# Optimization experiments

Measured on AMD Instinct MI355X. Metric: run time of the kernel, lower is better.

The kernel has to match this reference:

```python
import jax, jax.numpy as jnp
import numpy as np

N_NODES = 100000
N_EDGES = 800000


def gcn_conv(x, W, b, src, dst, ew, n):
    # PyG GCNConv with edge weights and self-loops already included in (src, dst, ew):
    # deg[i] = sum of incoming edge weights at i; norm_e = d^-1/2[src] * w_e * d^-1/2[dst]
    h = x @ W                                                  # [N, F_out]
    deg = jax.ops.segment_sum(ew, dst, num_segments=n)         # [N]
    dinv = jnp.where(deg > 0, jax.lax.rsqrt(deg), 0.0)
    norm = dinv[src] * ew * dinv[dst]                          # [E]
    out = jax.ops.segment_sum(h[src] * norm[:, None], dst, num_segments=n)
    return out + b


def add_self_loops(edge_index, edge_weight, n):
    loop = jnp.arange(n, dtype=edge_index.dtype)
    src = jnp.concatenate([edge_index[0], loop])
    dst = jnp.concatenate([edge_index[1], loop])
    ew = jnp.concatenate([edge_weight, jnp.ones((n,), edge_weight.dtype)])
    return src, dst, ew


def setup_inputs() -> dict:
    key = jax.random.key(0)
    ks = jax.random.split(key, 10)
    x = jax.random.normal(ks[0], (N_NODES, 5), jnp.float32)
    edge_index = jax.random.randint(ks[1], (2, N_EDGES), 0, N_NODES, dtype=jnp.int64)
    edge_weight = jax.random.uniform(ks[2], (N_EDGES,), jnp.float32)
    def glorot(k, fan_in, fan_out):
        s = float(np.sqrt(6.0 / (fan_in + fan_out)))
        return jax.random.uniform(k, (fan_in, fan_out), jnp.float32, -s, s)
    return {
        "x": x,
        "edge_index": edge_index,
        "edge_weight": edge_weight,
        "W1": glorot(ks[3], 5, 320),
        "b1": jnp.zeros((320,), jnp.float32),
        "W2": glorot(ks[4], 320, 160),
        "b2": jnp.zeros((160,), jnp.float32),
        "We": glorot(ks[5], 160, 80),
        "be": jnp.zeros((80,), jnp.float32),
    }


def reference(x, edge_index, edge_weight, W1, b1, W2, b2, We, be):
    n = x.shape[0]
    src, dst, ew = add_self_loops(edge_index, edge_weight, n)
    h = gcn_conv(x, W1, b1, src, dst, ew, n)        # conv1
    h = jax.nn.relu(h)
    h = gcn_conv(h, W2, b2, src, dst, ew, n)        # conv2
    return h @ We + be                              # embed linear
```

## Files before the change

kernel.cpp:

```cpp
#include <hip/hip_runtime.h>

#define NF0 5
#define F1 320
#define F2 160
#define F3 80
#define NSUB 8
#define SUBCAP 512

typedef float f32x4 __attribute__((ext_vector_type(4)));
typedef _Float16 f16x8 __attribute__((ext_vector_type(8)));


__global__ void k_init(int* __restrict__ zreg, int zwords,
                       const unsigned int* __restrict__ ei32, int E, int* __restrict__ flag) {
    for (int t = blockIdx.x * 256 + threadIdx.x; t < zwords; t += gridDim.x * 256)
        zreg[t] = 0;
    if (blockIdx.x == 0) {
        __shared__ int ok;
        if (threadIdx.x == 0) ok = 1;
        __syncthreads();
        int np = E < 2048 ? E : 2048;
        for (int i = threadIdx.x; i < np; i += 256)
            if (ei32[2 * i + 1] != 0u) ok = 0;
        __syncthreads();
        if (threadIdx.x == 0) *flag = ok;
    }
}


__global__ void k_binA(const void* ei, const float* __restrict__ ew, const int* __restrict__ flag,
                       int* __restrict__ bin_cnt , int2* __restrict__ bins,
                       int n_bins, int* __restrict__ ovf_n, int* __restrict__ ovf,
                       int ovf_cap, int E) {
    int e = blockIdx.x * blockDim.x + threadIdx.x;
    if (e >= E) return;
    int sub = blockIdx.x & (NSUB - 1);
    int s, d;
    if (*flag) {
        const long long* p = (const long long*)ei;
        s = (int)p[e]; d = (int)p[E + e];
    } else {
        const int* p = (const int*)ei;
        s = p[e]; d = p[E + e];
    }
    float w = ew[e];
    int b = d >> 8;
    int pos = atomicAdd(&bin_cnt[(sub * n_bins + b) * 4], 1);
    if (pos < SUBCAP) {
        int2 pk;
        pk.x = s | ((d & 255) << 24);
        pk.y = __float_as_int(w);
        bins[(size_t)b * (NSUB * SUBCAP) + sub * SUBCAP + pos] = pk;
    } else {
        int o = atomicAdd(ovf_n, 1);
        if (o < ovf_cap) {
            ovf[3 * o] = s; ovf[3 * o + 1] = d; ovf[3 * o + 2] = __float_as_int(w);
        }
    }
}


__global__ __launch_bounds__(512) void k_binB1x(const int2* __restrict__ bins,
                                                const int* __restrict__ bin_cnt, int n_bins,
                                                float* __restrict__ dinv,
                                                const int* __restrict__ ovf_n,
                                                const int* __restrict__ ovf, int ovf_cap, int N,
                                                const float* __restrict__ W2,
                                                const float* __restrict__ We,
                                                _Float16* __restrict__ Bh,
                                                const float* __restrict__ b2,
                                                const float* __restrict__ be,
                                                float* __restrict__ bc) {
    __shared__ float deg_l[256];
    int b = blockIdx.x, t = threadIdx.x;
    if (b >= n_bins) {
        int xb = b - n_bins;
        if (xb < 50) {
            int idx = xb * 512 + t;
            int fid = idx >> 9;
            int rem = idx & 511;
            int lane = rem >> 3, i = rem & 7;
            int kk = fid / 5, ct = fid - kk * 5;
            int col = ct * 16 + (lane & 15);
            int row = kk * 32 + (lane >> 4) * 8 + i;
            const float* wr = W2 + (size_t)row * F2;
            float acc = 0.f;
            #pragma unroll 4
            for (int m = 0; m < F2; m += 4) {
                float4 w4 = *(const float4*)(wr + m);
                acc += w4.x * We[m * F3 + col] + w4.y * We[(m + 1) * F3 + col]
                     + w4.z * We[(m + 2) * F3 + col] + w4.w * We[(m + 3) * F3 + col];
            }
            Bh[((size_t)fid * 64 + lane) * 8 + i] = (_Float16)acc;
        } else {
            if (t < F3) {
                float s = be[t];
                for (int k = 0; k < F2; ++k) s += b2[k] * We[k * F3 + t];
                bc[t] = s;
            }
        }
        return;
    }
    if (t < 256) deg_l[t] = 0.f;
    __syncthreads();
    int th = t >> 8;
    int tt = t & 255;
    for (int sp = 0; sp < NSUB; sp += 2) {
        int sub = sp + th;
        int ne = bin_cnt[(sub * n_bins + b) * 4]; if (ne > SUBCAP) ne = SUBCAP;
        const int2* bp = bins + (size_t)b * (NSUB * SUBCAP) + sub * SUBCAP;
        for (int j = tt; j < ne; j += 256) {
            int2 pk = bp[j];
            atomicAdd(&deg_l[((unsigned int)pk.x) >> 24], __int_as_float(pk.y));
        }
    }
    int n = *ovf_n; if (n > ovf_cap) n = ovf_cap;
    int lo = b * 256;
    for (int j = t; j < n; j += 512) {
        int d = ovf[3 * j + 1];
        if (d >= lo && d < lo + 256)
            atomicAdd(&deg_l[d - lo], __int_as_float(ovf[3 * j + 2]));
    }
    __syncthreads();
    int node = lo + t;
    if (t < 256 && node < N) dinv[node] = rsqrtf(1.0f + deg_l[t]);
}


__global__ __launch_bounds__(512) void k_binB2node(const int2* __restrict__ bins,
                                                   const int* __restrict__ bin_cnt, int n_bins,
                                                   const float* __restrict__ dinv,
                                                   const float* __restrict__ x,
                                                   const float* __restrict__ W1,
                                                   const float* __restrict__ b1,
                                                   const _Float16* __restrict__ Bh,
                                                   int* __restrict__ cnt,
                                                   int2* __restrict__ bucket, int cap,
                                                   int* __restrict__ ovf_n, int* __restrict__ ovf,
                                                   int ovf_cap,
                                                   _Float16* __restrict__ g, int N) {
    __shared__ int cnt_l[256];
    __shared__ float acc_l[256 * NF0];
    __shared__ float W_l[6 * F1];
    __shared__ _Float16 B_l[50 * 64 * 8];
    int b = blockIdx.x, t = threadIdx.x;

    if (t < 480) {
        float4 v = (t < 400) ? ((const float4*)W1)[t] : ((const float4*)b1)[t - 400];
        ((float4*)W_l)[t] = v;
    }
    {
        const float4* src = (const float4*)Bh;
        float4* dst = (float4*)B_l;
        for (int i = t; i < 3200; i += 512) dst[i] = src[i];
    }
    if (t < 256) cnt_l[t] = 0;
    for (int q = t; q < 256 * NF0; q += 512) acc_l[q] = 0.f;
    int nsnap = *ovf_n; if (nsnap > ovf_cap) nsnap = ovf_cap;
    __syncthreads();
    int lo = b * 256;

    for (int j = t; j < nsnap; j += 512) {
        int d = ovf[3 * j + 1];
        if (d >= lo && d < lo + 256) {
            int s = ovf[3 * j];
            float w = __int_as_float(ovf[3 * j + 2]) * dinv[s];
            const float* xs = x + (size_t)s * NF0;
            int dl = d - lo;
            #pragma unroll
            for (int f = 0; f < NF0; ++f)
                atomicAdd(&acc_l[dl * NF0 + f], xs[f] * w);
        }
    }

    int th = t >> 8;
    int tt = t & 255;
    for (int sp = 0; sp < NSUB; sp += 2) {
        int sub = sp + th;
        int ne = bin_cnt[(sub * n_bins + b) * 4]; if (ne > SUBCAP) ne = SUBCAP;
        const int2* bp = bins + (size_t)b * (NSUB * SUBCAP) + sub * SUBCAP;
        for (int j = tt; j < ne; j += 256) {
            int2 pk = bp[j];
            int s = pk.x & 0xFFFFFF;
            int dl = ((unsigned int)pk.x) >> 24;
            int node = lo + dl;
            int pos = atomicAdd(&cnt_l[dl], 1);
            if (pos < cap) {
                int2 out_pk; out_pk.x = s; out_pk.y = pk.y;
                bucket[(size_t)node * cap + pos] = out_pk;
            } else {
                int o = atomicAdd(ovf_n, 1);
                if (o < ovf_cap) { ovf[3 * o] = s; ovf[3 * o + 1] = node; ovf[3 * o + 2] = pk.y; }
            }
            float w = __int_as_float(pk.y) * dinv[s];
            const float* xs = x + (size_t)s * NF0;
            float4 sv = *(const float4*)xs;
            float s4 = xs[4];
            atomicAdd(&acc_l[dl * NF0 + 0], sv.x * w);
            atomicAdd(&acc_l[dl * NF0 + 1], sv.y * w);
            atomicAdd(&acc_l[dl * NF0 + 2], sv.z * w);
            atomicAdd(&acc_l[dl * NF0 + 3], sv.w * w);
            atomicAdd(&acc_l[dl * NF0 + 4], s4 * w);
        }
    }
    __syncthreads();

    int node0 = lo + t;
    if (t < 256 && node0 < N) {
        float di = dinv[node0];
        float sc = di * di;
        const float* xn = x + (size_t)node0 * NF0;
        #pragma unroll
        for (int f = 0; f < NF0; ++f)
            acc_l[t * NF0 + f] = di * acc_l[t * NF0 + f] + sc * xn[f];
        int c = cnt_l[t]; if (c > cap) c = cap;
        cnt[node0] = c;
    }
    __syncthreads();

    int w = t >> 6, l = t & 63;
    int nl = l & 15, kg = l >> 4;
    f32x4 zero = {0.f, 0.f, 0.f, 0.f};
    const f16x8* blp = (const f16x8*)B_l;

    #pragma unroll
    for (int set = 0; set < 2; ++set) {
        int nlocal = w * 32 + set * 16 + nl;
        int base = lo + w * 32 + set * 16;
        float a0v[5];
        #pragma unroll
        for (int j = 0; j < 5; ++j) a0v[j] = acc_l[nlocal * NF0 + j];

        f32x4 acc[5] = {zero, zero, zero, zero, zero};
        #pragma unroll
        for (int kk = 0; kk < 10; ++kk) {
            int k0 = kk * 32 + kg * 8;
            float v0[8];
            const float* bb = W_l + 5 * F1 + k0;
            #pragma unroll
            for (int i = 0; i < 8; ++i) v0[i] = bb[i];
            #pragma unroll
            for (int j = 0; j < 5; ++j) {
                const float* wp = W_l + j * F1 + k0;
                float aj0 = a0v[j];
                #pragma unroll
                for (int i = 0; i < 8; ++i) v0[i] += aj0 * wp[i];
            }
            f16x8 ah0;
            #pragma unroll
            for (int i = 0; i < 8; ++i)
                ah0[i] = (_Float16)fmaxf(v0[i], 0.f);
            #pragma unroll
            for (int ct = 0; ct < 5; ++ct) {
                f16x8 bf = blp[(kk * 5 + ct) * 64 + l];
                acc[ct] = __builtin_amdgcn_mfma_f32_16x16x32_f16(ah0, bf, acc[ct], 0, 0, 0);
            }
        }

        #pragma unroll
        for (int r = 0; r < 4; ++r) {
            int r0 = base + kg * 4 + r;
            if (r0 < N) {
                float dv = dinv[r0];
                #pragma unroll
                for (int ct = 0; ct < 5; ++ct)
                    g[(size_t)r0 * F3 + ct * 16 + nl] = (_Float16)(acc[ct][r] * dv);
            }
        }
    }
}


__global__ __launch_bounds__(256) void k_aggB(const _Float16* __restrict__ g,
                                              const float* __restrict__ dinv,
                                              const float* __restrict__ bc,
                                              const int* __restrict__ cnt,
                                              const int2* __restrict__ bucket, int cap,
                                              float* __restrict__ out, int N) {
    int t = blockIdx.x * blockDim.x + threadIdx.x;
    if (t >= 10 * N) return;
    int i = t / 10;
    int c = (t - i * 10) << 3;
    float acc[8];
    #pragma unroll
    for (int e = 0; e < 8; ++e) acc[e] = 0.f;
    int cn = cnt[i];
    const int4* row4 = (const int4*)(bucket + (size_t)i * cap);
    int j = 0;
    for (; j + 2 <= cn; j += 2) {
        int4 q = row4[j >> 1];
        float w0 = __int_as_float(q.y);
        float w1 = __int_as_float(q.w);
        f16x8 a0 = *(const f16x8*)(g + (size_t)q.x * F3 + c);
        f16x8 a1 = *(const f16x8*)(g + (size_t)q.z * F3 + c);
        #pragma unroll
        for (int e = 0; e < 8; ++e)
            acc[e] += (float)a0[e] * w0 + (float)a1[e] * w1;
    }
    if (j < cn) {
        int2 p0 = ((const int2*)row4)[j];
        float w0 = __int_as_float(p0.y);
        f16x8 a0 = *(const f16x8*)(g + (size_t)p0.x * F3 + c);
        #pragma unroll
        for (int e = 0; e < 8; ++e)
            acc[e] += (float)a0[e] * w0;
    }
    float di = dinv[i];
    f16x8 u0 = *(const f16x8*)(g + (size_t)i * F3 + c);
    const f32x4* bp = (const f32x4*)(bc + c);
    f32x4 q0 = bp[0], q1 = bp[1];
    f32x4 o0, o1;
    o0.x = di * (acc[0] + (float)u0[0]) + q0.x;
    o0.y = di * (acc[1] + (float)u0[1]) + q0.y;
    o0.z = di * (acc[2] + (float)u0[2]) + q0.z;
    o0.w = di * (acc[3] + (float)u0[3]) + q0.w;
    o1.x = di * (acc[4] + (float)u0[4]) + q1.x;
    o1.y = di * (acc[5] + (float)u0[5]) + q1.y;
    o1.z = di * (acc[6] + (float)u0[6]) + q1.z;
    o1.w = di * (acc[7] + (float)u0[7]) + q1.w;
    f32x4* op = (f32x4*)(out + (size_t)i * F3 + c);
    __builtin_nontemporal_store(o0, op);
    __builtin_nontemporal_store(o1, op + 1);
}

__global__ void k_fixB(const _Float16* __restrict__ g, const float* __restrict__ dinv,
                       const int* __restrict__ ovf_n, const int* __restrict__ ovf, int ovf_cap,
                       float* __restrict__ out) {
    int n = *ovf_n; if (n > ovf_cap) n = ovf_cap;
    for (int j = blockIdx.x * blockDim.x + threadIdx.x; j < n; j += gridDim.x * blockDim.x) {
        int s = ovf[3 * j], d = ovf[3 * j + 1];
        float w = dinv[d] * __int_as_float(ovf[3 * j + 2]);
        for (int f = 0; f < F3; ++f)
            atomicAdd(&out[(size_t)d * F3 + f], (float)g[(size_t)s * F3 + f] * w);
    }
}


static inline size_t align256(size_t x) { return (x + 255) & ~(size_t)255; }

extern "C" void kernel_launch(void* const* d_in, const int* in_sizes, int n_in,
                              void* d_out, int out_size, void* d_ws, size_t ws_size,
                              hipStream_t stream) {
    const float* x  = (const float*)d_in[0];
    const void*  ei = d_in[1];
    const float* ew = (const float*)d_in[2];
    const float* W1 = (const float*)d_in[3];
    const float* b1 = (const float*)d_in[4];
    const float* W2 = (const float*)d_in[5];
    const float* b2 = (const float*)d_in[6];
    const float* We = (const float*)d_in[7];
    const float* be = (const float*)d_in[8];
    float* out = (float*)d_out;

    int N = in_sizes[0] / NF0;
    int E = in_sizes[2];

    const int OVF_CAP = 131072;
    int n_bins = (N + 255) >> 8;

    char* p = (char*)d_ws;
    auto alloc = [&](size_t bytes) { char* r = p; p += align256(bytes); return r; };
    int*   flag  = (int*)alloc(4);
    int zwords = 16 + NSUB * n_bins * 4;
    int*   zreg  = (int*)alloc((size_t)zwords * 4);
    int*   ovf_n = zreg;
    int*   bin_cnt = zreg + 16;
    float* dinv  = (float*)alloc((size_t)N * 4);
    int*   cnt   = (int*)  alloc((size_t)N * 4);
    int*   ovf   = (int*)  alloc((size_t)OVF_CAP * 12);
    int2*  bins  = (int2*) alloc((size_t)n_bins * NSUB * SUBCAP * 8);
    float* bc    = (float*)alloc((size_t)F3 * 4);
    _Float16* Bh = (_Float16*)alloc((size_t)50 * 64 * 8 * 2);
    _Float16* g  = (_Float16*)alloc((size_t)N * F3 * 2);

    size_t used = (size_t)(p - (char*)d_ws);
    int cap = 24;
    if (ws_size > used) {
        size_t avail = (ws_size - used) / ((size_t)N * 8);
        if (avail < (size_t)cap) cap = (int)avail;
    } else cap = 4;
    cap &= ~1;
    if (cap < 4) cap = 4;
    int2* bucket = (int2*)alloc((size_t)N * cap * 8);

    int eb   = (E + 255) / 256;
    int zb   = (zwords + 255) / 256;

    k_init<<<zb, 256, 0, stream>>>(zreg, zwords, (const unsigned int*)ei, E, flag);
    k_binA<<<eb, 256, 0, stream>>>(ei, ew, flag, bin_cnt, bins, n_bins, ovf_n, ovf, OVF_CAP, E);
    k_binB1x<<<n_bins + 51, 512, 0, stream>>>(bins, bin_cnt, n_bins, dinv, ovf_n, ovf, OVF_CAP, N,
                                              W2, We, Bh, b2, be, bc);
    k_binB2node<<<n_bins, 512, 0, stream>>>(bins, bin_cnt, n_bins, dinv, x, W1, b1, Bh,
                                            cnt, bucket, cap, ovf_n, ovf, OVF_CAP, g, N);
    k_aggB<<<(10 * N + 255) / 256, 256, 0, stream>>>(g, dinv, bc, cnt, bucket, cap, out, N);
    k_fixB<<<16, 256, 0, stream>>>(g, dinv, ovf_n, ovf, OVF_CAP, out);
}
```

Measured before the change: 161.1 us.

## Split binning from node MLP kernel and fold overflow fixup into aggregation

The fused bin-scatter plus node-transform kernel is split in two. k_binB2 does the edge bucketing and layer-1 aggregation and writes an agg1 buffer; a new k_node kernel loads the weights into shared memory and runs the MFMA transform over 128-node tiles. The aim is to stop the roughly 59KB of weight staging in shared memory from limiting occupancy of the atomic-heavy scatter phase. The separate k_fixB atomic kernel is removed, and each k_aggB thread now scans the overflow list itself. The cost is an extra intermediate buffer round trip, and a per-thread linear scan that becomes expensive if overflow is large.

```diff
diff --git a/kernel.cpp b/kernel.cpp
--- a/kernel.cpp
+++ b/kernel.cpp
@@ -127,33 +127,17 @@
 }
 
 
-__global__ __launch_bounds__(512) void k_binB2node(const int2* __restrict__ bins,
-                                                   const int* __restrict__ bin_cnt, int n_bins,
-                                                   const float* __restrict__ dinv,
-                                                   const float* __restrict__ x,
-                                                   const float* __restrict__ W1,
-                                                   const float* __restrict__ b1,
-                                                   const _Float16* __restrict__ Bh,
-                                                   int* __restrict__ cnt,
-                                                   int2* __restrict__ bucket, int cap,
-                                                   int* __restrict__ ovf_n, int* __restrict__ ovf,
-                                                   int ovf_cap,
-                                                   _Float16* __restrict__ g, int N) {
+__global__ __launch_bounds__(512) void k_binB2(const int2* __restrict__ bins,
+                                               const int* __restrict__ bin_cnt, int n_bins,
+                                               const float* __restrict__ dinv,
+                                               const float* __restrict__ x,
+                                               int* __restrict__ cnt, int2* __restrict__ bucket,
+                                               int cap, float* __restrict__ agg1,
+                                               int* __restrict__ ovf_n, int* __restrict__ ovf,
+                                               int ovf_cap, int N) {
     __shared__ int cnt_l[256];
     __shared__ float acc_l[256 * NF0];
-    __shared__ float W_l[6 * F1];
-    __shared__ _Float16 B_l[50 * 64 * 8];
     int b = blockIdx.x, t = threadIdx.x;
-
-    if (t < 480) {
-        float4 v = (t < 400) ? ((const float4*)W1)[t] : ((const float4*)b1)[t - 400];
-        ((float4*)W_l)[t] = v;
-    }
-    {
-        const float4* src = (const float4*)Bh;
-        float4* dst = (float4*)B_l;
-        for (int i = t; i < 3200; i += 512) dst[i] = src[i];
-    }
     if (t < 256) cnt_l[t] = 0;
     for (int q = t; q < 256 * NF0; q += 512) acc_l[q] = 0.f;
     int nsnap = *ovf_n; if (nsnap > ovf_cap) nsnap = ovf_cap;
@@ -205,67 +189,90 @@
     }
     __syncthreads();
 
-    int node0 = lo + t;
-    if (t < 256 && node0 < N) {
-        float di = dinv[node0];
+    int node = lo + t;
+    if (t < 256 && node < N) {
+        float di = dinv[node];
         float sc = di * di;
-        const float* xn = x + (size_t)node0 * NF0;
+        const float* xn = x + (size_t)node * NF0;
+        float* op = agg1 + (size_t)node * NF0;
         #pragma unroll
         for (int f = 0; f < NF0; ++f)
-            acc_l[t * NF0 + f] = di * acc_l[t * NF0 + f] + sc * xn[f];
+            op[f] = di * acc_l[t * NF0 + f] + sc * xn[f];
         int c = cnt_l[t]; if (c > cap) c = cap;
-        cnt[node0] = c;
+        cnt[node] = c;
+    }
+}
+
+
+__global__ __launch_bounds__(512) void k_node(const float* __restrict__ agg1,
+                                              const float* __restrict__ W1,
+                                              const float* __restrict__ b1,
+                                              const _Float16* __restrict__ Bh,
+                                              const float* __restrict__ dinv,
+                                              _Float16* __restrict__ g, int N) {
+    __shared__ float W_l[6 * F1];
+    __shared__ _Float16 B_l[50 * 64 * 8];
+    int tid = threadIdx.x;
+    if (tid < 480) {
+        float4 v = (tid < 400) ? ((const float4*)W1)[tid] : ((const float4*)b1)[tid - 400];
+        ((float4*)W_l)[tid] = v;
+    }
+    {
+        const float4* src = (const float4*)Bh;
+        float4* dst = (float4*)B_l;
+        for (int i = tid; i < 3200; i += 512) dst[i] = src[i];
     }
     __syncthreads();
 
-    int w = t >> 6, l = t & 63;
+    int w = tid >> 6, l = tid & 63;
     int nl = l & 15, kg = l >> 4;
+    int base = blockIdx.x * 128 + w * 16;
+    int n0 = base + nl;
+
+    float a0v[5] = {0.f, 0.f, 0.f, 0.f, 0.f};
+    if (n0 < N) {
+        const float* ap = agg1 + (size_t)n0 * NF0;
+        #pragma unroll
+        for (int j = 0; j < 5; ++j) a0v[j] = ap[j];
+    }
+
     f32x4 zero = {0.f, 0.f, 0.f, 0.f};
+    f32x4 acc[5] = {zero, zero, zero, zero, zero};
     const f16x8* blp = (const f16x8*)B_l;
 
     #pragma unroll
-    for (int set = 0; set < 2; ++set) {
-        int nlocal = w * 32 + set * 16 + nl;
-        int base = lo + w * 32 + set * 16;
-        float a0v[5];
-        #pragma unroll
-        for (int j = 0; j < 5; ++j) a0v[j] = acc_l[nlocal * NF0 + j];
-
-        f32x4 acc[5] = {zero, zero, zero, zero, zero};
-        #pragma unroll
-        for (int kk = 0; kk < 10; ++kk) {
-            int k0 = kk * 32 + kg * 8;
-            float v0[8];
-            const float* bb = W_l + 5 * F1 + k0;
+    for (int kk = 0; kk < 10; ++kk) {
+        int k0 = kk * 32 + kg * 8;
+        float v0[8];
+        const float* bb = W_l + 5 * F1 + k0;
+        #pragma unroll
+        for (int i = 0; i < 8; ++i) v0[i] = bb[i];
+        #pragma unroll
+        for (int j = 0; j < 5; ++j) {
+            const float* wp = W_l + j * F1 + k0;
+            float aj0 = a0v[j];
             #pragma unroll
-            for (int i = 0; i < 8; ++i) v0[i] = bb[i];
+            for (int i = 0; i < 8; ++i) v0[i] += aj0 * wp[i];
+        }
+        f16x8 ah0;
+        #pragma unroll
+        for (int i = 0; i < 8; ++i)
+            ah0[i] = (_Float16)fmaxf(v0[i], 0.f);
+        #pragma unroll
+        for (int ct = 0; ct < 5; ++ct) {
+            f16x8 bf = blp[(kk * 5 + ct) * 64 + l];
+            acc[ct] = __builtin_amdgcn_mfma_f32_16x16x32_f16(ah0, bf, acc[ct], 0, 0, 0);
+        }
+    }
+
+    #pragma unroll
+    for (int r = 0; r < 4; ++r) {
+        int r0 = base + kg * 4 + r;
+        if (r0 < N) {
+            float dv = dinv[r0];
             #pragma unroll
-            for (int j = 0; j < 5; ++j) {
-                const float* wp = W_l + j * F1 + k0;
-                float aj0 = a0v[j];
-                #pragma unroll
-                for (int i = 0; i < 8; ++i) v0[i] += aj0 * wp[i];
-            }
-            f16x8 ah0;
-            #pragma unroll
-            for (int i = 0; i < 8; ++i)
-                ah0[i] = (_Float16)fmaxf(v0[i], 0.f);
-            #pragma unroll
-            for (int ct = 0; ct < 5; ++ct) {
-                f16x8 bf = blp[(kk * 5 + ct) * 64 + l];
-                acc[ct] = __builtin_amdgcn_mfma_f32_16x16x32_f16(ah0, bf, acc[ct], 0, 0, 0);
-            }
-        }
-
-        #pragma unroll
-        for (int r = 0; r < 4; ++r) {
-            int r0 = base + kg * 4 + r;
-            if (r0 < N) {
-                float dv = dinv[r0];
-                #pragma unroll
-                for (int ct = 0; ct < 5; ++ct)
-                    g[(size_t)r0 * F3 + ct * 16 + nl] = (_Float16)(acc[ct][r] * dv);
-            }
+            for (int ct = 0; ct < 5; ++ct)
+                g[(size_t)r0 * F3 + ct * 16 + nl] = (_Float16)(acc[ct][r] * dv);
         }
     }
 }
@@ -276,6 +283,8 @@
                                               const float* __restrict__ bc,
                                               const int* __restrict__ cnt,
                                               const int2* __restrict__ bucket, int cap,
+                                              const int* __restrict__ ovf_n,
+                                              const int* __restrict__ ovf, int ovf_cap,
                                               float* __restrict__ out, int N) {
     int t = blockIdx.x * blockDim.x + threadIdx.x;
     if (t >= 10 * N) return;
@@ -305,6 +314,19 @@
         for (int e = 0; e < 8; ++e)
             acc[e] += (float)a0[e] * w0;
     }
+    {
+        int n = *ovf_n; if (n > ovf_cap) n = ovf_cap;
+        for (int o = 0; o < n; ++o) {
+            if (ovf[3 * o + 1] == i) {
+                int s = ovf[3 * o];
+                float w0 = __int_as_float(ovf[3 * o + 2]);
+                f16x8 a0 = *(const f16x8*)(g + (size_t)s * F3 + c);
+                #pragma unroll
+                for (int e = 0; e < 8; ++e)
+                    acc[e] += (float)a0[e] * w0;
+            }
+        }
+    }
     float di = dinv[i];
     f16x8 u0 = *(const f16x8*)(g + (size_t)i * F3 + c);
     const f32x4* bp = (const f32x4*)(bc + c);
@@ -323,18 +345,6 @@
     __builtin_nontemporal_store(o1, op + 1);
 }
 
-__global__ void k_fixB(const _Float16* __restrict__ g, const float* __restrict__ dinv,
-                       const int* __restrict__ ovf_n, const int* __restrict__ ovf, int ovf_cap,
-                       float* __restrict__ out) {
-    int n = *ovf_n; if (n > ovf_cap) n = ovf_cap;
-    for (int j = blockIdx.x * blockDim.x + threadIdx.x; j < n; j += gridDim.x * blockDim.x) {
-        int s = ovf[3 * j], d = ovf[3 * j + 1];
-        float w = dinv[d] * __int_as_float(ovf[3 * j + 2]);
-        for (int f = 0; f < F3; ++f)
-            atomicAdd(&out[(size_t)d * F3 + f], (float)g[(size_t)s * F3 + f] * w);
-    }
-}
-
 
 static inline size_t align256(size_t x) { return (x + 255) & ~(size_t)255; }
 
@@ -369,6 +379,7 @@
     int*   cnt   = (int*)  alloc((size_t)N * 4);
     int*   ovf   = (int*)  alloc((size_t)OVF_CAP * 12);
     int2*  bins  = (int2*) alloc((size_t)n_bins * NSUB * SUBCAP * 8);
+    float* agg1  = (float*)alloc((size_t)N * NF0 * 4);
     float* bc    = (float*)alloc((size_t)F3 * 4);
     _Float16* Bh = (_Float16*)alloc((size_t)50 * 64 * 8 * 2);
     _Float16* g  = (_Float16*)alloc((size_t)N * F3 * 2);
@@ -390,8 +401,9 @@
     k_binA<<<eb, 256, 0, stream>>>(ei, ew, flag, bin_cnt, bins, n_bins, ovf_n, ovf, OVF_CAP, E);
     k_binB1x<<<n_bins + 51, 512, 0, stream>>>(bins, bin_cnt, n_bins, dinv, ovf_n, ovf, OVF_CAP, N,
                                               W2, We, Bh, b2, be, bc);
-    k_binB2node<<<n_bins, 512, 0, stream>>>(bins, bin_cnt, n_bins, dinv, x, W1, b1, Bh,
-                                            cnt, bucket, cap, ovf_n, ovf, OVF_CAP, g, N);
-    k_aggB<<<(10 * N + 255) / 256, 256, 0, stream>>>(g, dinv, bc, cnt, bucket, cap, out, N);
-    k_fixB<<<16, 256, 0, stream>>>(g, dinv, ovf_n, ovf, OVF_CAP, out);
-}
+    k_binB2<<<n_bins, 512, 0, stream>>>(bins, bin_cnt, n_bins, dinv, x, cnt, bucket, cap,
+                                        agg1, ovf_n, ovf, OVF_CAP, N);
+    k_node<<<(N + 127) / 128, 512, 0, stream>>>(agg1, W1, b1, Bh, dinv, g, N);
+    k_aggB<<<(10 * N + 255) / 256, 256, 0, stream>>>(g, dinv, bc, cnt, bucket, cap,
+                                                     ovf_n, ovf, OVF_CAP, out, N);
+}
```

Result: faster. 155.2 us (-3.7%).
